# Performance work log

Measured on AMD Instinct MI355X. Metric: run time of the kernel, lower is better.

Reference implementation:

```python
import jax, jax.numpy as jnp
import numpy as np

N = 4096
D_MODEL = 512


def setup_inputs() -> dict:
    key = jax.random.key(0)
    ks = jax.random.split(key, 5)
    scale = 1.0 / np.sqrt(D_MODEL)
    return {
        "x": jax.random.normal(ks[0], (N, D_MODEL), dtype=jnp.float32),
        "Wq": jax.random.normal(ks[1], (D_MODEL, D_MODEL), dtype=jnp.float32) * scale,
        "Wk": jax.random.normal(ks[2], (D_MODEL, D_MODEL), dtype=jnp.float32) * scale,
        "Wv": jax.random.normal(ks[3], (D_MODEL, D_MODEL), dtype=jnp.float32) * scale,
        "Ws": jax.random.normal(ks[4], (1, D_MODEL), dtype=jnp.float32) * scale,
    }


def reference(x, Wq, Wk, Wv, Ws):
    # x: [N, d]; torch nn.Linear(bias=False) computes x @ W.T
    Q = x @ Wq.T  # [N, d]
    K = x @ Wk.T  # [N, d]
    V = x @ Wv.T  # [N, d]
    sigma = jnp.clip(x @ Ws.T, 0.001, 1.0)  # [N, 1]

    # prior association: Gaussian kernel over |i - j| with per-row sigma
    pos = jnp.arange(sigma.shape[0], dtype=jnp.float32)
    diff = jnp.abs(pos[:, None] - pos[None, :])  # [N, N]
    gaussian = jnp.exp(-0.5 * (diff / sigma) ** 2) / jnp.sqrt(2.0 * jnp.pi * sigma)
    P = gaussian / (gaussian.sum(axis=1, keepdims=True) + 1e-8)

    scale = jnp.sqrt(jnp.float32(x.shape[-1]))
    S = jax.nn.softmax((Q @ K.T) / scale, axis=-1)  # [N, N]
    Z = S @ V  # [N, d]
    return Z, P, S
```

## Files before the change

kernel.cpp:

```cpp
#include <hip/hip_runtime.h>
#include <math.h>

#define N_TOK 4096
#define DM 512

typedef _Float16 f16x8 __attribute__((ext_vector_type(8)));
typedef _Float16 f16x4 __attribute__((ext_vector_type(4)));
typedef float f32x4 __attribute__((ext_vector_type(4)));

__device__ __forceinline__ void async_ld16(const ushort* g, ushort* l) {
  __builtin_amdgcn_global_load_lds(
      (const __attribute__((address_space(1))) void*)g,
      (__attribute__((address_space(3))) void*)l, 16, 0, 0);
}

__global__ __launch_bounds__(256) void pack_sigma(
    const float* __restrict__ x, const float* __restrict__ Wq,
    const float* __restrict__ Wk, const float* __restrict__ Wv,
    const float* __restrict__ Ws, _Float16* __restrict__ x16,
    _Float16* __restrict__ Wc16, float* __restrict__ sg) {
  const int b = blockIdx.x;
  const int t = threadIdx.x;
  if (b < 2048) {
    int i = b * 1024 + t * 4;
    float4 v = *(const float4*)&x[i];
    f16x4 o;
    o.x = (_Float16)v.x; o.y = (_Float16)v.y;
    o.z = (_Float16)v.z; o.w = (_Float16)v.w;
    *(f16x4*)&x16[i] = o;
    int col = (t * 4) & 511;
    float4 w = *(const float4*)&Ws[col];
    float p = v.x * w.x + v.y * w.y + v.z * w.z + v.w * w.w;
    __shared__ float red[256];
    red[t] = p;
    __syncthreads();
    int lt = t & 127;
    for (int off = 64; off > 0; off >>= 1) {
      if (lt < off) red[t] += red[t + off];
      __syncthreads();
    }
    if (lt == 0) {
      float s = red[t];
      sg[2 * b + (t >> 7)] = fminf(fmaxf(s, 0.001f), 1.0f);
    }
  } else {
    int e = (b - 2048) * 1024 + t * 4;
    const float* src;
    int le = e & (DM * DM - 1);
    if (e < DM * DM) src = Wq + le;
    else if (e < 2 * DM * DM) src = Wk + le;
    else src = Wv + le;
    float4 v = *(const float4*)src;
    f16x4 o;
    o.x = (_Float16)v.x; o.y = (_Float16)v.y;
    o.z = (_Float16)v.z; o.w = (_Float16)v.w;
    *(f16x4*)&Wc16[e] = o;
  }
}

template <int EPI>
__global__ __launch_bounds__(256) void mfma_f16(
    const _Float16* __restrict__ A, int lda, const _Float16* __restrict__ B,
    int ldb, int K, float scale, float* __restrict__ Cf, int ldc,
    _Float16* __restrict__ D0, _Float16* __restrict__ D1,
    _Float16* __restrict__ D2, float* __restrict__ Part) {
  __shared__ _Float16 lds[2 * 128 * 32];
  _Float16* Ah = lds;
  _Float16* Bh = lds + 128 * 32;

  const int t = threadIdx.x;
  const int w = t >> 6, L = t & 63;
  const int wm = (w >> 1) * 64, wn = (w & 1) * 64;
  const int row = L & 15, quad = L >> 4;
  const int bm = blockIdx.y * 128, bn = blockIdx.x * 128;
  const int kbase = blockIdx.z * K;

  f32x4 acc[4][4] = {{}};

  const int c0 = t, c1 = t + 256;
  const int r0 = c0 >> 2, o0 = (c0 & 3) * 8;
  const int r1 = r0 + 64;

  const ushort* ga0 = (const ushort*)(A + (size_t)(bm + r0) * lda + kbase + o0);
  const ushort* ga1 = (const ushort*)(A + (size_t)(bm + r1) * lda + kbase + o0);
  const ushort* gb0 = (const ushort*)(B + (size_t)(bn + r0) * ldb + kbase + o0);
  const ushort* gb1 = (const ushort*)(B + (size_t)(bn + r1) * ldb + kbase + o0);

  for (int k0 = 0; k0 < K; k0 += 32) {
    async_ld16(ga0, (ushort*)(Ah + c0 * 8));
    async_ld16(ga1, (ushort*)(Ah + c1 * 8));
    async_ld16(gb0, (ushort*)(Bh + c0 * 8));
    async_ld16(gb1, (ushort*)(Bh + c1 * 8));
    ga0 += 32; ga1 += 32; gb0 += 32; gb1 += 32;
    __syncthreads();

    f16x8 a0[4], b0[4];
#pragma unroll
    for (int i = 0; i < 4; ++i)
      a0[i] = *(const f16x8*)&Ah[(wm + i * 16 + row) * 32 + quad * 8];
#pragma unroll
    for (int j = 0; j < 4; ++j)
      b0[j] = *(const f16x8*)&Bh[(wn + j * 16 + row) * 32 + quad * 8];
#pragma unroll
    for (int i = 0; i < 4; ++i)
#pragma unroll
      for (int j = 0; j < 4; ++j)
        acc[i][j] = __builtin_amdgcn_mfma_f32_16x16x32_f16(a0[i], b0[j],
                                                           acc[i][j], 0, 0, 0);
    __syncthreads();
  }

  if (EPI == 1) {
    const int region = bn >> 9;
    _Float16* D = (region == 0) ? D0 : ((region == 1) ? D1 : D2);
#pragma unroll
    for (int i = 0; i < 4; ++i)
#pragma unroll
      for (int j = 0; j < 4; ++j)
#pragma unroll
        for (int r = 0; r < 4; ++r) {
          int gr = bm + wm + i * 16 + quad * 4 + r;
          int nn = (bn & 511) + wn + j * 16 + row;
          D[(size_t)gr * 512 + nn] = (_Float16)acc[i][j][r];
        }
  } else if (EPI == 3) {
#pragma unroll
    for (int i = 0; i < 4; ++i)
#pragma unroll
      for (int j = 0; j < 4; ++j)
#pragma unroll
        for (int r = 0; r < 4; ++r) {
          int gr = bm + wm + i * 16 + quad * 4 + r;
          int gc = bn + wn + j * 16 + row;
          D0[(size_t)gr * ldc + gc] = (_Float16)(acc[i][j][r] * scale);
        }
  } else {
    const int z = blockIdx.z;
    float* dst = (z == 0) ? Cf : (Part + (size_t)(z - 1) * 2097152);
#pragma unroll
    for (int i = 0; i < 4; ++i)
#pragma unroll
      for (int j = 0; j < 4; ++j)
#pragma unroll
        for (int r = 0; r < 4; ++r) {
          int gr = bm + wm + i * 16 + quad * 4 + r;
          int gc = bn + wn + j * 16 + row;
          dst[(size_t)gr * ldc + gc] = acc[i][j][r] * scale;
        }
  }
}

__global__ __launch_bounds__(256) void transpose16(
    const _Float16* __restrict__ V16, _Float16* __restrict__ VT) {
  __shared__ _Float16 T[32][34];
  const int t = threadIdx.x;
  const int r = t >> 3, c4 = (t & 7) * 4;
  f16x4 v = *(const f16x4*)&V16[(size_t)(blockIdx.y * 32 + r) * 512 +
                                blockIdx.x * 32 + c4];
  T[r][c4] = v.x; T[r][c4 + 1] = v.y; T[r][c4 + 2] = v.z; T[r][c4 + 3] = v.w;
  __syncthreads();
  f16x4 o;
  o.x = T[c4][r]; o.y = T[c4 + 1][r]; o.z = T[c4 + 2][r]; o.w = T[c4 + 3][r];
  *(f16x4*)&VT[(size_t)(blockIdx.x * 32 + r) * 4096 + blockIdx.y * 32 + c4] = o;
}

__global__ __launch_bounds__(256) void softmax_kernel(
    _Float16* __restrict__ Sc, float* __restrict__ S) {
  __shared__ float red[256];
  const int t = threadIdx.x;
  _Float16* Srow16 = Sc + (size_t)blockIdx.x * N_TOK;
  float* Srow = S + (size_t)blockIdx.x * N_TOK;
  float f[16];
  float m = -INFINITY;
#pragma unroll
  for (int r = 0; r < 4; ++r) {
    f16x4 h = *(const f16x4*)&Srow16[r * 1024 + t * 4];
    f[r * 4 + 0] = (float)h.x; f[r * 4 + 1] = (float)h.y;
    f[r * 4 + 2] = (float)h.z; f[r * 4 + 3] = (float)h.w;
    m = fmaxf(m, fmaxf(fmaxf(f[r * 4], f[r * 4 + 1]),
                       fmaxf(f[r * 4 + 2], f[r * 4 + 3])));
  }
  red[t] = m;
  __syncthreads();
  for (int off = 128; off > 0; off >>= 1) {
    if (t < off) red[t] = fmaxf(red[t], red[t + off]);
    __syncthreads();
  }
  m = red[0];
  __syncthreads();
  float sum = 0.f;
#pragma unroll
  for (int i = 0; i < 16; ++i) {
    f[i] = __expf(f[i] - m);
    sum += f[i];
  }
  red[t] = sum;
  __syncthreads();
  for (int off = 128; off > 0; off >>= 1) {
    if (t < off) red[t] += red[t + off];
    __syncthreads();
  }
  const float inv = 1.0f / red[0];
#pragma unroll
  for (int r = 0; r < 4; ++r) {
    float4 o;
    o.x = f[r * 4 + 0] * inv; o.y = f[r * 4 + 1] * inv;
    o.z = f[r * 4 + 2] * inv; o.w = f[r * 4 + 3] * inv;
    *(float4*)&Srow[r * 1024 + t * 4] = o;
    f16x4 h;
    h.x = (_Float16)o.x; h.y = (_Float16)o.y;
    h.z = (_Float16)o.z; h.w = (_Float16)o.w;
    *(f16x4*)&Srow16[r * 1024 + t * 4] = h;
  }
}

__global__ __launch_bounds__(256) void tail_kernel(
    const float* __restrict__ sigma, float* __restrict__ P,
    float* __restrict__ Z, const float* __restrict__ Part) {
  const int t = threadIdx.x;
  if (blockIdx.x >= 4096) {
    int i = (blockIdx.x - 4096) * 1024 + t * 4;
    float4 z = *(const float4*)&Z[i];
    float4 a = *(const float4*)&Part[i];
    float4 b = *(const float4*)&Part[2097152 + i];
    float4 c = *(const float4*)&Part[2 * 2097152 + i];
    z.x += a.x + b.x + c.x;
    z.y += a.y + b.y + c.y;
    z.z += a.z + b.z + c.z;
    z.w += a.w + b.w + c.w;
    *(float4*)&Z[i] = z;
    return;
  }
  __shared__ float red[256];
  const int i = blockIdx.x;
  const float sg = sigma[i];
  const float inv2 = -0.5f / (sg * sg);
  const float c = rsqrtf(6.283185307179586f * sg);
  float4 g[4];
  float sum = 0.f;
#pragma unroll
  for (int r = 0; r < 4; ++r) {
    int j = r * 1024 + t * 4;
    float d0 = (float)(i - j);
    float d1 = (float)(i - j - 1);
    float d2 = (float)(i - j - 2);
    float d3 = (float)(i - j - 3);
    g[r].x = __expf(inv2 * d0 * d0) * c;
    g[r].y = __expf(inv2 * d1 * d1) * c;
    g[r].z = __expf(inv2 * d2 * d2) * c;
    g[r].w = __expf(inv2 * d3 * d3) * c;
    sum += g[r].x + g[r].y + g[r].z + g[r].w;
  }
  red[t] = sum;
  __syncthreads();
  for (int off = 128; off > 0; off >>= 1) {
    if (t < off) red[t] += red[t + off];
    __syncthreads();
  }
  const float inv = 1.0f / (red[0] + 1e-8f);
  float* Prow = P + (size_t)i * N_TOK;
#pragma unroll
  for (int r = 0; r < 4; ++r) {
    g[r].x *= inv; g[r].y *= inv; g[r].z *= inv; g[r].w *= inv;
    *(float4*)&Prow[r * 1024 + t * 4] = g[r];
  }
}

extern "C" void kernel_launch(void* const* d_in, const int* in_sizes, int n_in,
                              void* d_out, int out_size, void* d_ws,
                              size_t ws_size, hipStream_t stream) {
  const float* x = (const float*)d_in[0];
  const float* Wq = (const float*)d_in[1];
  const float* Wk = (const float*)d_in[2];
  const float* Wv = (const float*)d_in[3];
  const float* Ws = (const float*)d_in[4];

  float* out = (float*)d_out;
  float* Z = out;
  float* Pout = Z + (size_t)N_TOK * DM;
  float* S = Pout + (size_t)N_TOK * N_TOK;

  const size_t E = (size_t)N_TOK * DM;
  _Float16* Q16 = (_Float16*)Pout;
  _Float16* K16 = Q16 + E;
  _Float16* V16 = K16 + E;
  _Float16* VT16 = V16 + E;
  _Float16* Sc16 = VT16 + E;

  _Float16* x16 = (_Float16*)d_ws;
  _Float16* Wc16 = x16 + E;
  float* sg = (float*)(Wc16 + 3 * DM * DM);
  float* Part = sg + 4096;

  const dim3 blk(256);

  pack_sigma<<<2816, blk, 0, stream>>>(x, Wq, Wk, Wv, Ws, x16, Wc16, sg);

  mfma_f16<1><<<dim3(12, 32), blk, 0, stream>>>(
      x16, DM, Wc16, DM, DM, 1.0f, nullptr, 0, Q16, K16, V16, nullptr);

  transpose16<<<dim3(16, 128), blk, 0, stream>>>(V16, VT16);

  mfma_f16<3><<<dim3(32, 32), blk, 0, stream>>>(
      Q16, DM, K16, DM, DM, 1.0f / sqrtf((float)DM), nullptr, N_TOK, Sc16,
      nullptr, nullptr, nullptr);

  softmax_kernel<<<N_TOK, blk, 0, stream>>>(Sc16, S);

  mfma_f16<2><<<dim3(4, 32, 4), blk, 0, stream>>>(
      Sc16, N_TOK, VT16, N_TOK, N_TOK / 4, 1.0f, Z, DM, nullptr, nullptr,
      nullptr, Part);

  tail_kernel<<<4096 + 2048, blk, 0, stream>>>(sg, Pout, Z, Part);
}
```

Baseline: 262.0 us.

## Fuse softmax exponent and row sums into QK^T epilogue, defer normalization

```diff
diff --git a/kernel.cpp b/kernel.cpp
--- a/kernel.cpp
+++ b/kernel.cpp
@@ -18,7 +18,8 @@
     const float* __restrict__ x, const float* __restrict__ Wq,
     const float* __restrict__ Wk, const float* __restrict__ Wv,
     const float* __restrict__ Ws, _Float16* __restrict__ x16,
-    _Float16* __restrict__ Wc16, float* __restrict__ sg) {
+    _Float16* __restrict__ Wc16, float* __restrict__ sg,
+    float* __restrict__ denom) {
   const int b = blockIdx.x;
   const int t = threadIdx.x;
   if (b < 2048) {
@@ -43,7 +44,7 @@
       float s = red[t];
       sg[2 * b + (t >> 7)] = fminf(fmaxf(s, 0.001f), 1.0f);
     }
-  } else {
+  } else if (b < 2816) {
     int e = (b - 2048) * 1024 + t * 4;
     const float* src;
     int le = e & (DM * DM - 1);
@@ -55,6 +56,10 @@
     o.x = (_Float16)v.x; o.y = (_Float16)v.y;
     o.z = (_Float16)v.z; o.w = (_Float16)v.w;
     *(f16x4*)&Wc16[e] = o;
+  } else {
+    float4 zz = {0.f, 0.f, 0.f, 0.f};
+#pragma unroll
+    for (int k = 0; k < 4; ++k) *(float4*)&denom[(t * 4 + k * 1024)] = zz;
   }
 }
 
@@ -63,8 +68,10 @@
     const _Float16* __restrict__ A, int lda, const _Float16* __restrict__ B,
     int ldb, int K, float scale, float* __restrict__ Cf, int ldc,
     _Float16* __restrict__ D0, _Float16* __restrict__ D1,
-    _Float16* __restrict__ D2, float* __restrict__ Part) {
+    _Float16* __restrict__ D2, _Float16* __restrict__ Part16,
+    float* __restrict__ denom) {
   __shared__ _Float16 lds[2 * 128 * 32];
+  __shared__ float dinv[128];
   _Float16* Ah = lds;
   _Float16* Bh = lds + 128 * 32;
 
@@ -74,6 +81,8 @@
   const int row = L & 15, quad = L >> 4;
   const int bm = blockIdx.y * 128, bn = blockIdx.x * 128;
   const int kbase = blockIdx.z * K;
+
+  if (EPI == 2 && t < 128) dinv[t] = 1.0f / denom[bm + t];
 
   f32x4 acc[4][4] = {{}};
 
@@ -123,29 +132,43 @@
           int nn = (bn & 511) + wn + j * 16 + row;
           D[(size_t)gr * 512 + nn] = (_Float16)acc[i][j][r];
         }
-  } else if (EPI == 3) {
-#pragma unroll
-    for (int i = 0; i < 4; ++i)
-#pragma unroll
-      for (int j = 0; j < 4; ++j)
-#pragma unroll
-        for (int r = 0; r < 4; ++r) {
-          int gr = bm + wm + i * 16 + quad * 4 + r;
+  } else if (EPI == 4) {
+#pragma unroll
+    for (int i = 0; i < 4; ++i)
+#pragma unroll
+      for (int r = 0; r < 4; ++r) {
+        int gr = bm + wm + i * 16 + quad * 4 + r;
+        float s = 0.f;
+#pragma unroll
+        for (int j = 0; j < 4; ++j) {
+          float e = __expf(acc[i][j][r] * scale);
           int gc = bn + wn + j * 16 + row;
-          D0[(size_t)gr * ldc + gc] = (_Float16)(acc[i][j][r] * scale);
+          D0[(size_t)gr * ldc + gc] = (_Float16)e;
+          s += e;
         }
+        s += __shfl_xor(s, 1);
+        s += __shfl_xor(s, 2);
+        s += __shfl_xor(s, 4);
+        s += __shfl_xor(s, 8);
+        if (row == 0) atomicAdd(&denom[gr], s);
+      }
   } else {
     const int z = blockIdx.z;
-    float* dst = (z == 0) ? Cf : (Part + (size_t)(z - 1) * 2097152);
 #pragma unroll
     for (int i = 0; i < 4; ++i)
 #pragma unroll
       for (int j = 0; j < 4; ++j)
 #pragma unroll
         for (int r = 0; r < 4; ++r) {
-          int gr = bm + wm + i * 16 + quad * 4 + r;
+          int lr = wm + i * 16 + quad * 4 + r;
+          int gr = bm + lr;
           int gc = bn + wn + j * 16 + row;
-          dst[(size_t)gr * ldc + gc] = acc[i][j][r] * scale;
+          float v = acc[i][j][r] * dinv[lr];
+          if (z == 0)
+            Cf[(size_t)gr * ldc + gc] = v;
+          else
+            Part16[(size_t)(z - 1) * 2097152 + (size_t)gr * ldc + gc] =
+                (_Float16)v;
         }
   }
 }
@@ -164,75 +187,39 @@
   *(f16x4*)&VT[(size_t)(blockIdx.x * 32 + r) * 4096 + blockIdx.y * 32 + c4] = o;
 }
 
-__global__ __launch_bounds__(256) void softmax_kernel(
-    _Float16* __restrict__ Sc, float* __restrict__ S) {
-  __shared__ float red[256];
-  const int t = threadIdx.x;
-  _Float16* Srow16 = Sc + (size_t)blockIdx.x * N_TOK;
-  float* Srow = S + (size_t)blockIdx.x * N_TOK;
-  float f[16];
-  float m = -INFINITY;
-#pragma unroll
-  for (int r = 0; r < 4; ++r) {
-    f16x4 h = *(const f16x4*)&Srow16[r * 1024 + t * 4];
-    f[r * 4 + 0] = (float)h.x; f[r * 4 + 1] = (float)h.y;
-    f[r * 4 + 2] = (float)h.z; f[r * 4 + 3] = (float)h.w;
-    m = fmaxf(m, fmaxf(fmaxf(f[r * 4], f[r * 4 + 1]),
-                       fmaxf(f[r * 4 + 2], f[r * 4 + 3])));
-  }
-  red[t] = m;
-  __syncthreads();
-  for (int off = 128; off > 0; off >>= 1) {
-    if (t < off) red[t] = fmaxf(red[t], red[t + off]);
-    __syncthreads();
-  }
-  m = red[0];
-  __syncthreads();
-  float sum = 0.f;
-#pragma unroll
-  for (int i = 0; i < 16; ++i) {
-    f[i] = __expf(f[i] - m);
-    sum += f[i];
-  }
-  red[t] = sum;
-  __syncthreads();
-  for (int off = 128; off > 0; off >>= 1) {
-    if (t < off) red[t] += red[t + off];
-    __syncthreads();
-  }
-  const float inv = 1.0f / red[0];
-#pragma unroll
-  for (int r = 0; r < 4; ++r) {
-    float4 o;
-    o.x = f[r * 4 + 0] * inv; o.y = f[r * 4 + 1] * inv;
-    o.z = f[r * 4 + 2] * inv; o.w = f[r * 4 + 3] * inv;
-    *(float4*)&Srow[r * 1024 + t * 4] = o;
-    f16x4 h;
-    h.x = (_Float16)o.x; h.y = (_Float16)o.y;
-    h.z = (_Float16)o.z; h.w = (_Float16)o.w;
-    *(f16x4*)&Srow16[r * 1024 + t * 4] = h;
-  }
-}
-
 __global__ __launch_bounds__(256) void tail_kernel(
     const float* __restrict__ sigma, float* __restrict__ P,
-    float* __restrict__ Z, const float* __restrict__ Part) {
+    float* __restrict__ Z, const _Float16* __restrict__ Part16,
+    const _Float16* __restrict__ E16, const float* __restrict__ denom,
+    float* __restrict__ S) {
   const int t = threadIdx.x;
-  if (blockIdx.x >= 4096) {
-    int i = (blockIdx.x - 4096) * 1024 + t * 4;
+  const int b = blockIdx.x;
+  if (b >= 6144) {
+    int idx = (b - 6144) * 1024 + t * 4;
+    int rw = (b - 6144) >> 2;
+    float inv = 1.0f / denom[rw];
+    f16x4 e = *(const f16x4*)&E16[idx];
+    float4 o;
+    o.x = (float)e.x * inv; o.y = (float)e.y * inv;
+    o.z = (float)e.z * inv; o.w = (float)e.w * inv;
+    *(float4*)&S[idx] = o;
+    return;
+  }
+  if (b >= 4096) {
+    int i = (b - 4096) * 1024 + t * 4;
     float4 z = *(const float4*)&Z[i];
-    float4 a = *(const float4*)&Part[i];
-    float4 b = *(const float4*)&Part[2097152 + i];
-    float4 c = *(const float4*)&Part[2 * 2097152 + i];
-    z.x += a.x + b.x + c.x;
-    z.y += a.y + b.y + c.y;
-    z.z += a.z + b.z + c.z;
-    z.w += a.w + b.w + c.w;
+    f16x4 a = *(const f16x4*)&Part16[i];
+    f16x4 c = *(const f16x4*)&Part16[2097152 + i];
+    f16x4 d = *(const f16x4*)&Part16[2 * 2097152 + i];
+    z.x += (float)a.x + (float)c.x + (float)d.x;
+    z.y += (float)a.y + (float)c.y + (float)d.y;
+    z.z += (float)a.z + (float)c.z + (float)d.z;
+    z.w += (float)a.w + (float)c.w + (float)d.w;
     *(float4*)&Z[i] = z;
     return;
   }
   __shared__ float red[256];
-  const int i = blockIdx.x;
+  const int i = b;
   const float sg = sigma[i];
   const float inv2 = -0.5f / (sg * sg);
   const float c = rsqrtf(6.283185307179586f * sg);
@@ -285,31 +272,31 @@
   _Float16* K16 = Q16 + E;
   _Float16* V16 = K16 + E;
   _Float16* VT16 = V16 + E;
-  _Float16* Sc16 = VT16 + E;
 
   _Float16* x16 = (_Float16*)d_ws;
   _Float16* Wc16 = x16 + E;
   float* sg = (float*)(Wc16 + 3 * DM * DM);
-  float* Part = sg + 4096;
+  float* denom = sg + 4096;
+  _Float16* Part16 = (_Float16*)(denom + 4096);
+  _Float16* E16 = Part16 + 3 * E;
 
   const dim3 blk(256);
 
-  pack_sigma<<<2816, blk, 0, stream>>>(x, Wq, Wk, Wv, Ws, x16, Wc16, sg);
+  pack_sigma<<<2817, blk, 0, stream>>>(x, Wq, Wk, Wv, Ws, x16, Wc16, sg, denom);
 
   mfma_f16<1><<<dim3(12, 32), blk, 0, stream>>>(
-      x16, DM, Wc16, DM, DM, 1.0f, nullptr, 0, Q16, K16, V16, nullptr);
+      x16, DM, Wc16, DM, DM, 1.0f, nullptr, 0, Q16, K16, V16, nullptr, nullptr);
 
   transpose16<<<dim3(16, 128), blk, 0, stream>>>(V16, VT16);
 
-  mfma_f16<3><<<dim3(32, 32), blk, 0, stream>>>(
-      Q16, DM, K16, DM, DM, 1.0f / sqrtf((float)DM), nullptr, N_TOK, Sc16,
-      nullptr, nullptr, nullptr);
-
-  softmax_kernel<<<N_TOK, blk, 0, stream>>>(Sc16, S);
+  mfma_f16<4><<<dim3(32, 32), blk, 0, stream>>>(
+      Q16, DM, K16, DM, DM, 1.0f / sqrtf((float)DM), nullptr, N_TOK, E16,
+      nullptr, nullptr, nullptr, denom);
 
   mfma_f16<2><<<dim3(4, 32, 4), blk, 0, stream>>>(
-      Sc16, N_TOK, VT16, N_TOK, N_TOK / 4, 1.0f, Z, DM, nullptr, nullptr,
-      nullptr, Part);
-
-  tail_kernel<<<4096 + 2048, blk, 0, stream>>>(sg, Pout, Z, Part);
-}
+      E16, N_TOK, VT16, N_TOK, N_TOK / 4, 1.0f, Z, DM, nullptr, nullptr,
+      nullptr, Part16, denom);
+
+  tail_kernel<<<4096 + 2048 + 16384, blk, 0, stream>>>(sg, Pout, Z, Part16,
+                                                       E16, denom, S);
+}
```

New measurement: 264.7 us. Within noise of the previous version (+1.0%).
